# Kernel optimization log

Measured on AMD Instinct MI355X. Metric: run time of the kernel, lower is better.

Reference implementation:

```python
import jax, jax.numpy as jnp
import numpy as np

B, T, I, H, C = 128, 1024, 256, 512, 32

def setup_inputs() -> dict:
    key = jax.random.key(0)
    ks = jax.random.split(key, 10)
    x = jax.random.normal(ks[0], (B, T, I), dtype=jnp.float32)
    constraints = jax.random.normal(ks[1], (B, C), dtype=jnp.float32)
    lengths = jax.random.randint(ks[2], (B,), 1, T + 1, dtype=jnp.int32).at[0].set(T)
    s = 1.0 / np.sqrt(H)
    W_ih = jax.random.uniform(ks[3], (H, I), minval=-s, maxval=s, dtype=jnp.float32)
    b_ih = jax.random.uniform(ks[4], (H,), minval=-s, maxval=s, dtype=jnp.float32)
    W_hh = jax.random.uniform(ks[5], (H, H), minval=-s, maxval=s, dtype=jnp.float32)
    b_hh = jax.random.uniform(ks[6], (H,), minval=-s, maxval=s, dtype=jnp.float32)
    W_ch = jax.random.uniform(ks[7], (H, C), minval=-s, maxval=s, dtype=jnp.float32)
    b_ch = jax.random.uniform(ks[8], (H,), minval=-s, maxval=s, dtype=jnp.float32)
    return {"x": x, "constraints": constraints, "lengths": lengths,
            "W_ih": W_ih, "b_ih": b_ih, "W_hh": W_hh, "b_hh": b_hh,
            "W_ch": W_ch, "b_ch": b_ch}


def reference(x, constraints, lengths, W_ih, b_ih, W_hh, b_hh, W_ch, b_ch):
    # Packed variable-length RNN == masked scan over time (per-sequence math
    # is unaffected by pack/sort; padded positions output zeros, matching
    # pad_packed_sequence).
    Bn, Tn, _ = x.shape
    Hn = W_hh.shape[0]
    # Precompute all time-independent projections once.
    xp = jnp.einsum('bti,hi->tbh', x, W_ih) + b_ih            # [T,B,H]
    cp = constraints @ W_ch.T + b_ch + b_hh                   # [B,H]
    mask = jnp.arange(Tn)[:, None] < lengths[None, :]         # [T,B]

    def step(h, inp):
        xproj, m = inp
        h_new = jnp.tanh(xproj + cp + h @ W_hh.T)
        m = m[:, None]
        h = jnp.where(m, h_new, h)
        out = jnp.where(m, h_new, jnp.zeros((), x.dtype))
        return h, out

    h0 = jnp.zeros((Bn, Hn), x.dtype)
    _, outs = jax.lax.scan(step, h0, (xp, mask))              # outs: [T,B,H]
    outputs = jnp.transpose(outs, (1, 0, 2))                  # [B,T,H]
    last = outputs[jnp.arange(Bn), lengths - 1]               # [B,H]
    return outputs, last
```

## Files before the change

kernel.cpp:

```cpp
#include <hip/hip_runtime.h>
#include <hip/hip_bf16.h>

#define BB 128
#define TT 1024
#define II 256
#define HH 512
#define CC 32

#define KRR 8
#define KLL 4
#define KSS 4

typedef short bf16x8 __attribute__((ext_vector_type(8)));
typedef float f32x4 __attribute__((ext_vector_type(4)));

__device__ __forceinline__ unsigned short f2bf(float f) {
  union { __hip_bfloat16 h; unsigned short u; } cv;
  cv.h = __float2bfloat16(f);
  return cv.u;
}

__global__ void k_prep(const float* __restrict__ Whh, const float* __restrict__ Wih,
                       const float* __restrict__ cons, const float* __restrict__ Wch,
                       const float* __restrict__ bch, const float* __restrict__ bhh,
                       unsigned short* __restrict__ whh_bf, unsigned short* __restrict__ wih_bf,
                       float* __restrict__ cp) {
  int bid = blockIdx.x, tid = threadIdx.x;
  if (bid < 256) {
    int idx = bid * 1024 + tid * 4;
    float4 v = *reinterpret_cast<const float4*>(Whh + idx);
    ushort4 u = make_ushort4(f2bf(v.x), f2bf(v.y), f2bf(v.z), f2bf(v.w));
    *reinterpret_cast<ushort4*>(whh_bf + idx) = u;
  } else if (bid < 384) {
    int idx = (bid - 256) * 1024 + tid * 4;
    float4 v = *reinterpret_cast<const float4*>(Wih + idx);
    ushort4 u = make_ushort4(f2bf(v.x), f2bf(v.y), f2bf(v.z), f2bf(v.w));
    *reinterpret_cast<ushort4*>(wih_bf + idx) = u;
  } else {
    int b = bid - 384;
    for (int h = tid; h < HH; h += 256) {
      float s = bch[h] + bhh[h];
      #pragma unroll
      for (int c = 0; c < CC; ++c) s += cons[b * CC + c] * Wch[h * CC + c];
      cp[b * HH + h] = s;
    }
  }
}

__launch_bounds__(256, 2)
__global__ void k_xp(const float* __restrict__ x, const unsigned short* __restrict__ wih_bf,
                     const float* __restrict__ bih, float* __restrict__ out) {
  __shared__ unsigned short As[64 * 64];
  __shared__ unsigned short Ws[512 * 64];
  int tid = threadIdx.x;
  int w = tid >> 6, l = tid & 63, lo = l & 15, hi = l >> 4;
  int m0 = blockIdx.x * 64;

  f32x4 acc[32];
  #pragma unroll
  for (int i = 0; i < 32; ++i) acc[i] = (f32x4){0.f, 0.f, 0.f, 0.f};

  float bias[32];
  #pragma unroll
  for (int nt = 0; nt < 32; ++nt) bias[nt] = bih[nt * 16 + lo];

  char* Asc = reinterpret_cast<char*>(As);
  char* Wsc = reinterpret_cast<char*>(Ws);

  for (int kit = 0; kit < 4; ++kit) {
    int k0 = kit * 64;
    __syncthreads();
    {
      int r = tid >> 2;
      int kq = (tid & 3) * 16;
      const float* src = x + (long)(m0 + r) * II + k0 + kq;
      #pragma unroll
      for (int q = 0; q < 4; ++q) {
        float4 v = *reinterpret_cast<const float4*>(src + q * 4);
        ushort4 u = make_ushort4(f2bf(v.x), f2bf(v.y), f2bf(v.z), f2bf(v.w));
        int byte = ((kq + q * 4) * 2) ^ ((r & 7) << 4);
        *reinterpret_cast<ushort4*>(Asc + r * 128 + byte) = u;
      }
    }
    {
      int rr = tid >> 3;
      int cc = (tid & 7) * 8;
      #pragma unroll
      for (int p = 0; p < 16; ++p) {
        int r = p * 32 + rr;
        uint4 v = *reinterpret_cast<const uint4*>(wih_bf + r * II + k0 + cc);
        int byte = (cc * 2) ^ ((r & 7) << 4);
        *reinterpret_cast<uint4*>(Wsc + r * 128 + byte) = v;
      }
    }
    __syncthreads();
    #pragma unroll
    for (int kt = 0; kt < 2; ++kt) {
      int kbyte = kt * 64 + hi * 16;
      int arow = w * 16 + lo;
      bf16x8 af = *reinterpret_cast<const bf16x8*>(Asc + arow * 128 + (kbyte ^ ((arow & 7) << 4)));
      #pragma unroll
      for (int nt = 0; nt < 32; ++nt) {
        int brow = nt * 16 + lo;
        bf16x8 bfr = *reinterpret_cast<const bf16x8*>(Wsc + brow * 128 + (kbyte ^ ((brow & 7) << 4)));
        acc[nt] = __builtin_amdgcn_mfma_f32_16x16x32_bf16(af, bfr, acc[nt], 0, 0, 0);
      }
    }
  }
  #pragma unroll
  for (int i = 0; i < 4; ++i) {
    float* dst = out + (long)(m0 + w * 16 + hi * 4 + i) * HH + lo;
    #pragma unroll
    for (int nt = 0; nt < 32; ++nt) dst[nt * 16] = acc[nt][i] + bias[nt];
  }
}

__launch_bounds__(512, 2)
__global__ void k_rnn(float* __restrict__ out,
                      const unsigned short* __restrict__ whh_bf,
                      const float* __restrict__ cp,
                      const int* __restrict__ lengths) {
  __shared__ unsigned short hbuf[16 * 512];
  __shared__ unsigned short wlds[8 * 4 * KLL * 512];
  int tid = threadIdx.x;
  int w = tid >> 6, l = tid & 63, lo = l & 15, hi = l >> 4;
  int bbase = blockIdx.x * 16;

  int ncol[4];
  #pragma unroll
  for (int nt = 0; nt < 4; ++nt) ncol[nt] = w * 64 + nt * 16 + lo;

  int len[4];
  #pragma unroll
  for (int i = 0; i < 4; ++i) len[i] = lengths[bbase + hi * 4 + i];

  float cpv[4][4];
  #pragma unroll
  for (int i = 0; i < 4; ++i)
    #pragma unroll
    for (int nt = 0; nt < 4; ++nt)
      cpv[i][nt] = cp[(bbase + hi * 4 + i) * HH + ncol[nt]];

  bf16x8 wreg[KRR][4];
  #pragma unroll
  for (int kt = 0; kt < KRR; ++kt)
    #pragma unroll
    for (int nt = 0; nt < 4; ++nt)
      wreg[kt][nt] = *reinterpret_cast<const bf16x8*>(whh_bf + ncol[nt] * HH + kt * 32 + hi * 8);

  #pragma unroll
  for (int kt = 0; kt < KLL; ++kt)
    #pragma unroll
    for (int nt = 0; nt < 4; ++nt) {
      bf16x8 v = *reinterpret_cast<const bf16x8*>(whh_bf + ncol[nt] * HH + (KRR + kt) * 32 + hi * 8);
      *reinterpret_cast<bf16x8*>(wlds + (((w * 4 + nt) * KLL + kt) * 64 + l) * 8) = v;
    }

  {
    bf16x8 z = {0, 0, 0, 0, 0, 0, 0, 0};
    *reinterpret_cast<bf16x8*>(hbuf + tid * 16) = z;
    *reinterpret_cast<bf16x8*>(hbuf + tid * 16 + 8) = z;
  }

  float* ptr[4];
  #pragma unroll
  for (int i = 0; i < 4; ++i)
    ptr[i] = out + (long)(bbase + hi * 4 + i) * TT * HH + ncol[0];

  char* hbc = reinterpret_cast<char*>(hbuf);
  long last_base = (long)BB * TT * HH;

  __syncthreads();

  #pragma unroll 1
  for (int t = 0; t < TT; ++t) {
    float xpv[4][4];
    #pragma unroll
    for (int i = 0; i < 4; ++i)
      #pragma unroll
      for (int nt = 0; nt < 4; ++nt)
        xpv[i][nt] = ptr[i][nt * 16];

    f32x4 acc[4];
    #pragma unroll
    for (int nt = 0; nt < 4; ++nt) acc[nt] = (f32x4){0.f, 0.f, 0.f, 0.f};

    bf16x8 wstr[KSS][4];
    #pragma unroll
    for (int kt = 0; kt < 16; ++kt) {
      if (kt >= KRR + KLL - 3 && kt < KRR + KLL - 3 + KSS) {
        int ks = kt - (KRR + KLL - 3);
        #pragma unroll
        for (int nt = 0; nt < 4; ++nt)
          wstr[ks][nt] = *reinterpret_cast<const bf16x8*>(
              whh_bf + ncol[nt] * HH + (KRR + KLL + ks) * 32 + hi * 8);
      }
      int abyte = (kt * 64 + hi * 16) ^ ((lo & 7) << 4);
      bf16x8 af = *reinterpret_cast<const bf16x8*>(hbc + lo * 1024 + abyte);
      #pragma unroll
      for (int nt = 0; nt < 4; ++nt) {
        bf16x8 bfr;
        if (kt < KRR)            bfr = wreg[kt][nt];
        else if (kt < KRR + KLL) bfr = *reinterpret_cast<const bf16x8*>(
                                         wlds + (((w * 4 + nt) * KLL + (kt - KRR)) * 64 + l) * 8);
        else                     bfr = wstr[kt - KRR - KLL][nt];
        acc[nt] = __builtin_amdgcn_mfma_f32_16x16x32_bf16(af, bfr, acc[nt], 0, 0, 0);
      }
    }
    __syncthreads();

    #pragma unroll
    for (int i = 0; i < 4; ++i) {
      bool valid = (t < len[i]);
      bool lastw = (t + 1 == len[i]);
      int brow = hi * 4 + i;
      #pragma unroll
      for (int nt = 0; nt < 4; ++nt) {
        float pre = acc[nt][i] + cpv[i][nt] + xpv[i][nt];
        pre = fminf(fmaxf(pre, -15.f), 15.f);
        float e = __expf(2.f * pre);
        float th = __builtin_fmaf(-2.f, __builtin_amdgcn_rcpf(e + 1.f), 1.f);
        ptr[i][nt * 16] = valid ? th : 0.f;
        if (valid) {
          int cbyte = (ncol[nt] * 2) ^ ((brow & 7) << 4);
          *reinterpret_cast<unsigned short*>(hbc + brow * 1024 + cbyte) = f2bf(th);
        }
        if (lastw) {
          out[last_base + (long)(bbase + brow) * HH + ncol[nt]] = th;
        }
      }
      ptr[i] += HH;
    }
    __syncthreads();
  }
}

extern "C" void kernel_launch(void* const* d_in, const int* in_sizes, int n_in,
                              void* d_out, int out_size, void* d_ws, size_t ws_size,
                              hipStream_t stream) {
  const float* x     = (const float*)d_in[0];
  const float* cons  = (const float*)d_in[1];
  const int*   lens  = (const int*)d_in[2];
  const float* W_ih  = (const float*)d_in[3];
  const float* b_ih  = (const float*)d_in[4];
  const float* W_hh  = (const float*)d_in[5];
  const float* b_hh  = (const float*)d_in[6];
  const float* W_ch  = (const float*)d_in[7];
  const float* b_ch  = (const float*)d_in[8];
  float* out = (float*)d_out;

  unsigned short* whh_bf = (unsigned short*)d_ws;
  unsigned short* wih_bf = (unsigned short*)((char*)d_ws + 512 * 1024);
  float*          cpbuf  = (float*)((char*)d_ws + 768 * 1024);

  k_prep<<<512, 256, 0, stream>>>(W_hh, W_ih, cons, W_ch, b_ch, b_hh, whh_bf, wih_bf, cpbuf);
  k_xp<<<2048, 256, 0, stream>>>(x, wih_bf, b_ih, out);
  k_rnn<<<8, 512, 0, stream>>>(out, whh_bf, cpbuf, lens);
}
```

Before: 7.059 ms.

## Double-buffer hidden state, transpose MFMA layout, fold constraint bias into projection

The recurrent kernel now double-buffers the bf16 hidden state in LDS, which removes one barrier per timestep. It keeps 12 of 16 weight k-tiles in registers and the rest in LDS, dropping the per-step global weight streaming. It also swaps MFMA operands so each lane owns one batch row and four contiguous columns, allowing float4 loads and stores of the xp/output rows. The constraint projection is folded into the input-projection kernel's epilogue, so the recurrence no longer adds it. Outputs are written from bf16-rounded tanh values and the clamp before tanh is removed, which lowers output precision and could risk overflow handling in exp.

```diff
diff --git a/kernel.cpp b/kernel.cpp
--- a/kernel.cpp
+++ b/kernel.cpp
@@ -7,9 +7,8 @@
 #define HH 512
 #define CC 32
 
-#define KRR 8
+#define KRR 12
 #define KLL 4
-#define KSS 4
 
 typedef short bf16x8 __attribute__((ext_vector_type(8)));
 typedef float f32x4 __attribute__((ext_vector_type(4)));
@@ -18,6 +17,16 @@
   union { __hip_bfloat16 h; unsigned short u; } cv;
   cv.h = __float2bfloat16(f);
   return cv.u;
+}
+__device__ __forceinline__ float bflo(unsigned int u) {
+  return __uint_as_float(u << 16);
+}
+__device__ __forceinline__ float bfhi(unsigned int u) {
+  return __uint_as_float(u & 0xffff0000u);
+}
+__device__ __forceinline__ float tanh_fast(float x) {
+  float e = __expf(2.f * x);
+  return __builtin_fmaf(-2.f, __builtin_amdgcn_rcpf(e + 1.f), 1.f);
 }
 
 __global__ void k_prep(const float* __restrict__ Whh, const float* __restrict__ Wih,
@@ -49,20 +58,18 @@
 
 __launch_bounds__(256, 2)
 __global__ void k_xp(const float* __restrict__ x, const unsigned short* __restrict__ wih_bf,
-                     const float* __restrict__ bih, float* __restrict__ out) {
+                     const float* __restrict__ bih, const float* __restrict__ cp,
+                     float* __restrict__ out) {
   __shared__ unsigned short As[64 * 64];
   __shared__ unsigned short Ws[512 * 64];
   int tid = threadIdx.x;
   int w = tid >> 6, l = tid & 63, lo = l & 15, hi = l >> 4;
   int m0 = blockIdx.x * 64;
+  int b = blockIdx.x >> 4;
 
   f32x4 acc[32];
   #pragma unroll
   for (int i = 0; i < 32; ++i) acc[i] = (f32x4){0.f, 0.f, 0.f, 0.f};
-
-  float bias[32];
-  #pragma unroll
-  for (int nt = 0; nt < 32; ++nt) bias[nt] = bih[nt * 16 + lo];
 
   char* Asc = reinterpret_cast<char*>(As);
   char* Wsc = reinterpret_cast<char*>(Ws);
@@ -103,25 +110,28 @@
       for (int nt = 0; nt < 32; ++nt) {
         int brow = nt * 16 + lo;
         bf16x8 bfr = *reinterpret_cast<const bf16x8*>(Wsc + brow * 128 + (kbyte ^ ((brow & 7) << 4)));
-        acc[nt] = __builtin_amdgcn_mfma_f32_16x16x32_bf16(af, bfr, acc[nt], 0, 0, 0);
-      }
-    }
-  }
-  #pragma unroll
-  for (int i = 0; i < 4; ++i) {
-    float* dst = out + (long)(m0 + w * 16 + hi * 4 + i) * HH + lo;
-    #pragma unroll
-    for (int nt = 0; nt < 32; ++nt) dst[nt * 16] = acc[nt][i] + bias[nt];
+        acc[nt] = __builtin_amdgcn_mfma_f32_16x16x32_bf16(bfr, af, acc[nt], 0, 0, 0);
+      }
+    }
+  }
+  long row = (long)(m0 + w * 16 + lo) * HH;
+  #pragma unroll
+  for (int nt = 0; nt < 32; ++nt) {
+    int col = nt * 16 + hi * 4;
+    float4 bb = *reinterpret_cast<const float4*>(bih + col);
+    float4 cc = *reinterpret_cast<const float4*>(cp + b * HH + col);
+    float4 o = make_float4(acc[nt][0] + bb.x + cc.x, acc[nt][1] + bb.y + cc.y,
+                           acc[nt][2] + bb.z + cc.z, acc[nt][3] + bb.w + cc.w);
+    *reinterpret_cast<float4*>(out + row + col) = o;
   }
 }
 
 __launch_bounds__(512, 2)
 __global__ void k_rnn(float* __restrict__ out,
                       const unsigned short* __restrict__ whh_bf,
-                      const float* __restrict__ cp,
                       const int* __restrict__ lengths) {
-  __shared__ unsigned short hbuf[16 * 512];
-  __shared__ unsigned short wlds[8 * 4 * KLL * 512];
+  __shared__ unsigned short hbuf[2][16 * 512];
+  __shared__ unsigned short wlds[8 * 4 * KLL * 64 * 8];
   int tid = threadIdx.x;
   int w = tid >> 6, l = tid & 63, lo = l & 15, hi = l >> 4;
   int bbase = blockIdx.x * 16;
@@ -129,24 +139,20 @@
   int ncol[4];
   #pragma unroll
   for (int nt = 0; nt < 4; ++nt) ncol[nt] = w * 64 + nt * 16 + lo;
-
-  int len[4];
-  #pragma unroll
-  for (int i = 0; i < 4; ++i) len[i] = lengths[bbase + hi * 4 + i];
-
-  float cpv[4][4];
-  #pragma unroll
-  for (int i = 0; i < 4; ++i)
-    #pragma unroll
-    for (int nt = 0; nt < 4; ++nt)
-      cpv[i][nt] = cp[(bbase + hi * 4 + i) * HH + ncol[nt]];
+  int c0[4];
+  #pragma unroll
+  for (int nt = 0; nt < 4; ++nt) c0[nt] = w * 64 + nt * 16 + hi * 4;
+
+  int len_b = lengths[bbase + lo];
 
   bf16x8 wreg[KRR][4];
   #pragma unroll
   for (int kt = 0; kt < KRR; ++kt)
     #pragma unroll
-    for (int nt = 0; nt < 4; ++nt)
+    for (int nt = 0; nt < 4; ++nt) {
       wreg[kt][nt] = *reinterpret_cast<const bf16x8*>(whh_bf + ncol[nt] * HH + kt * 32 + hi * 8);
+      asm volatile("" : "+v"(wreg[kt][nt]));
+    }
 
   #pragma unroll
   for (int kt = 0; kt < KLL; ++kt)
@@ -158,80 +164,84 @@
 
   {
     bf16x8 z = {0, 0, 0, 0, 0, 0, 0, 0};
-    *reinterpret_cast<bf16x8*>(hbuf + tid * 16) = z;
-    *reinterpret_cast<bf16x8*>(hbuf + tid * 16 + 8) = z;
-  }
-
-  float* ptr[4];
-  #pragma unroll
-  for (int i = 0; i < 4; ++i)
-    ptr[i] = out + (long)(bbase + hi * 4 + i) * TT * HH + ncol[0];
-
-  char* hbc = reinterpret_cast<char*>(hbuf);
-  long last_base = (long)BB * TT * HH;
+    *reinterpret_cast<bf16x8*>(&hbuf[0][tid * 16]) = z;
+    *reinterpret_cast<bf16x8*>(&hbuf[0][tid * 16 + 8]) = z;
+  }
+  uint2 ph[4];
+  #pragma unroll
+  for (int nt = 0; nt < 4; ++nt) ph[nt] = make_uint2(0u, 0u);
+
+  float* orow = out + (long)(bbase + lo) * TT * HH;
+  float* lastrow = out + (long)BB * TT * HH + (long)(bbase + lo) * HH;
+
+  const char* wc = reinterpret_cast<const char*>(wlds);
+  unsigned short* RB = &hbuf[0][0];
+  unsigned short* WB = &hbuf[1][0];
 
   __syncthreads();
 
   #pragma unroll 1
   for (int t = 0; t < TT; ++t) {
-    float xpv[4][4];
-    #pragma unroll
-    for (int i = 0; i < 4; ++i)
+    float4 xv[4];
+    #pragma unroll
+    for (int nt = 0; nt < 4; ++nt) xv[nt] = *reinterpret_cast<const float4*>(orow + c0[nt]);
+    __builtin_amdgcn_sched_barrier(0);
+
+    f32x4 acc[4];
+    #pragma unroll
+    for (int nt = 0; nt < 4; ++nt) acc[nt] = (f32x4){0.f, 0.f, 0.f, 0.f};
+    const char* rb = reinterpret_cast<const char*>(RB);
+    #pragma unroll
+    for (int kt = 0; kt < KRR; ++kt) {
+      int abyte = (kt * 64 + hi * 16) ^ ((lo & 7) << 4);
+      bf16x8 af = *reinterpret_cast<const bf16x8*>(rb + lo * 1024 + abyte);
       #pragma unroll
       for (int nt = 0; nt < 4; ++nt)
-        xpv[i][nt] = ptr[i][nt * 16];
-
-    f32x4 acc[4];
-    #pragma unroll
-    for (int nt = 0; nt < 4; ++nt) acc[nt] = (f32x4){0.f, 0.f, 0.f, 0.f};
-
-    bf16x8 wstr[KSS][4];
-    #pragma unroll
-    for (int kt = 0; kt < 16; ++kt) {
-      if (kt >= KRR + KLL - 3 && kt < KRR + KLL - 3 + KSS) {
-        int ks = kt - (KRR + KLL - 3);
-        #pragma unroll
-        for (int nt = 0; nt < 4; ++nt)
-          wstr[ks][nt] = *reinterpret_cast<const bf16x8*>(
-              whh_bf + ncol[nt] * HH + (KRR + KLL + ks) * 32 + hi * 8);
-      }
+        acc[nt] = __builtin_amdgcn_mfma_f32_16x16x32_bf16(wreg[kt][nt], af, acc[nt], 0, 0, 0);
+    }
+    #pragma unroll
+    for (int kt = KRR; kt < 16; ++kt) {
       int abyte = (kt * 64 + hi * 16) ^ ((lo & 7) << 4);
-      bf16x8 af = *reinterpret_cast<const bf16x8*>(hbc + lo * 1024 + abyte);
+      bf16x8 af = *reinterpret_cast<const bf16x8*>(rb + lo * 1024 + abyte);
       #pragma unroll
       for (int nt = 0; nt < 4; ++nt) {
-        bf16x8 bfr;
-        if (kt < KRR)            bfr = wreg[kt][nt];
-        else if (kt < KRR + KLL) bfr = *reinterpret_cast<const bf16x8*>(
-                                         wlds + (((w * 4 + nt) * KLL + (kt - KRR)) * 64 + l) * 8);
-        else                     bfr = wstr[kt - KRR - KLL][nt];
-        acc[nt] = __builtin_amdgcn_mfma_f32_16x16x32_bf16(af, bfr, acc[nt], 0, 0, 0);
-      }
+        bf16x8 bw = *reinterpret_cast<const bf16x8*>(
+            wc + (((w * 4 + nt) * KLL + (kt - KRR)) * 64 + l) * 16);
+        acc[nt] = __builtin_amdgcn_mfma_f32_16x16x32_bf16(bw, af, acc[nt], 0, 0, 0);
+      }
+    }
+
+    bool valid = (t < len_b);
+    bool lastw = (t + 1 == len_b);
+    uint2 thp[4];
+    char* wbp = reinterpret_cast<char*>(WB) + lo * 1024;
+    int swz = (lo & 7) << 4;
+    #pragma unroll
+    for (int nt = 0; nt < 4; ++nt) {
+      float t0 = tanh_fast(acc[nt][0] + xv[nt].x);
+      float t1 = tanh_fast(acc[nt][1] + xv[nt].y);
+      float t2 = tanh_fast(acc[nt][2] + xv[nt].z);
+      float t3 = tanh_fast(acc[nt][3] + xv[nt].w);
+      thp[nt].x = (unsigned int)f2bf(t0) | ((unsigned int)f2bf(t1) << 16);
+      thp[nt].y = (unsigned int)f2bf(t2) | ((unsigned int)f2bf(t3) << 16);
+      if (valid) ph[nt] = thp[nt];
+      *reinterpret_cast<uint2*>(wbp + ((w * 128 + nt * 32 + hi * 8) ^ swz)) = ph[nt];
     }
     __syncthreads();
 
     #pragma unroll
-    for (int i = 0; i < 4; ++i) {
-      bool valid = (t < len[i]);
-      bool lastw = (t + 1 == len[i]);
-      int brow = hi * 4 + i;
-      #pragma unroll
-      for (int nt = 0; nt < 4; ++nt) {
-        float pre = acc[nt][i] + cpv[i][nt] + xpv[i][nt];
-        pre = fminf(fmaxf(pre, -15.f), 15.f);
-        float e = __expf(2.f * pre);
-        float th = __builtin_fmaf(-2.f, __builtin_amdgcn_rcpf(e + 1.f), 1.f);
-        ptr[i][nt * 16] = valid ? th : 0.f;
-        if (valid) {
-          int cbyte = (ncol[nt] * 2) ^ ((brow & 7) << 4);
-          *reinterpret_cast<unsigned short*>(hbc + brow * 1024 + cbyte) = f2bf(th);
-        }
-        if (lastw) {
-          out[last_base + (long)(bbase + brow) * HH + ncol[nt]] = th;
-        }
-      }
-      ptr[i] += HH;
-    }
-    __syncthreads();
+    for (int nt = 0; nt < 4; ++nt) {
+      float4 o;
+      o.x = valid ? bflo(thp[nt].x) : 0.f;
+      o.y = valid ? bfhi(thp[nt].x) : 0.f;
+      o.z = valid ? bflo(thp[nt].y) : 0.f;
+      o.w = valid ? bfhi(thp[nt].y) : 0.f;
+      *reinterpret_cast<float4*>(orow + c0[nt]) = o;
+      if (lastw) *reinterpret_cast<float4*>(lastrow + c0[nt]) = o;
+    }
+
+    unsigned short* tmp = RB; RB = WB; WB = tmp;
+    orow += HH;
   }
 }
 
@@ -254,6 +264,6 @@
   float*          cpbuf  = (float*)((char*)d_ws + 768 * 1024);
 
   k_prep<<<512, 256, 0, stream>>>(W_hh, W_ih, cons, W_ch, b_ch, b_hh, whh_bf, wih_bf, cpbuf);
-  k_xp<<<2048, 256, 0, stream>>>(x, wih_bf, b_ih, out);
-  k_rnn<<<8, 512, 0, stream>>>(out, whh_bf, cpbuf, lens);
-}
+  k_xp<<<2048, 256, 0, stream>>>(x, wih_bf, b_ih, cpbuf, out);
+  k_rnn<<<8, 512, 0, stream>>>(out, whh_bf, lens);
+}
```

After: 5.658 ms. -19.8%, faster.
